# Performance work log

Measured on AMD Instinct MI355X. Metric: run time of the kernel, lower is better.

Reference implementation:

```python
import jax, jax.numpy as jnp
import numpy as np

HIDDEN = 768
HEADS = 12
HEAD_DIM = HIDDEN // HEADS
INTER = 1152
WINDOW = 128
EPS = 1e-5
ROPE_WAVELENGTH = 10000.0


def setup_inputs() -> dict:
    key = jax.random.key(0)
    ks = jax.random.split(key, 8)
    B, S = 2, 2048
    x = jax.random.normal(ks[0], (B, S, HIDDEN), dtype=jnp.float32)
    padding_mask = jnp.ones((B, S), dtype=jnp.int32)
    sc = 0.02
    wqkv = jax.random.normal(ks[1], (HIDDEN, 3 * HIDDEN), dtype=jnp.float32) * sc
    wo_attn = jax.random.normal(ks[2], (HIDDEN, HIDDEN), dtype=jnp.float32) * sc
    wi0 = jax.random.normal(ks[3], (HIDDEN, INTER), dtype=jnp.float32) * sc
    wi1 = jax.random.normal(ks[4], (HIDDEN, INTER), dtype=jnp.float32) * sc
    wo_mlp = jax.random.normal(ks[5], (INTER, HIDDEN), dtype=jnp.float32) * sc
    g_attn = jnp.ones((HIDDEN,), dtype=jnp.float32)
    g_mlp = jnp.ones((HIDDEN,), dtype=jnp.float32)
    return dict(x=x, padding_mask=padding_mask, wqkv=wqkv, wo_attn=wo_attn,
                wi0=wi0, wi1=wi1, wo_mlp=wo_mlp, g_attn=g_attn, g_mlp=g_mlp)


def _rmsnorm(x, gamma):
    # Keras LayerNormalization(rms_scaling=True): x * rsqrt(mean(x^2)+eps) * gamma
    inv = jax.lax.rsqrt(jnp.mean(jnp.square(x), axis=-1, keepdims=True) + EPS)
    return x * inv * gamma


def _rope(t):
    # t: [B, S, H, D]; standard rotate-half RoPE over the head dim
    S, D = t.shape[1], t.shape[3]
    inv_freq = 1.0 / (ROPE_WAVELENGTH ** (jnp.arange(0, D, 2, dtype=jnp.float32) / D))
    freqs = jnp.arange(S, dtype=jnp.float32)[:, None] * inv_freq[None, :]  # [S, D/2]
    emb = jnp.concatenate([freqs, freqs], axis=-1)  # [S, D]
    cos = jnp.cos(emb)[None, :, None, :]
    sin = jnp.sin(emb)[None, :, None, :]
    h1, h2 = jnp.split(t, 2, axis=-1)
    rot = jnp.concatenate([-h2, h1], axis=-1)
    return t * cos + rot * sin


def reference(x, padding_mask, wqkv, wo_attn, wi0, wi1, wo_mlp, g_attn, g_mlp):
    B, S, _ = x.shape
    # --- attention sub-block ---
    res = x
    h = _rmsnorm(x, g_attn)
    qkv = (h @ wqkv).reshape(B, S, 3, HEADS, HEAD_DIM)
    q, k, v = qkv[:, :, 0], qkv[:, :, 1], qkv[:, :, 2]  # [B, S, H, D]
    q = _rope(q)
    k = _rope(k)
    scores = jnp.einsum('bqhd,bkhd->bhqk', q, k) / jnp.sqrt(
        jnp.asarray(HEAD_DIM, x.dtype))
    pos = jnp.arange(S)
    window = (jnp.abs(pos[:, None] - pos[None, :]) <= WINDOW // 2).astype(jnp.float32)
    mask = window[None, None, :, :] * padding_mask.astype(jnp.float32)[:, None, None, :]
    scores = scores + (1.0 - mask) * -1e9
    attn = jax.nn.softmax(scores, axis=-1)
    out = jnp.einsum('bhqk,bkhd->bqhd', attn, v).reshape(B, S, HIDDEN)
    x = res + out @ wo_attn
    # --- GeGLU MLP sub-block ---
    res = x
    h = _rmsnorm(x, g_mlp)
    h = jax.nn.gelu(h @ wi0, approximate=True) * (h @ wi1)
    return res + h @ wo_mlp
```

## Files before the change

kernel.cpp:

```cpp
#include <hip/hip_runtime.h>
#include <hip/hip_bf16.h>

#define HID 768
#define NHEADS 12
#define HD 64
#define INTER 1152
#define SEQ 2048
#define NB 2
#define ROWS (NB * SEQ)
#define QTA 64
#define KTA 192

typedef __attribute__((ext_vector_type(8))) short bf16x8;
typedef __attribute__((ext_vector_type(4))) float f32x4;

__device__ __forceinline__ float bf2f(unsigned short u) {
    union { unsigned int i; float f; } c; c.i = ((unsigned int)u) << 16; return c.f;
}
__device__ __forceinline__ unsigned short f2bf(float f) {
    union { float f; unsigned int i; } c; c.f = f;
    unsigned int b = c.i;
    b += 0x7FFFu + ((b >> 16) & 1u);
    return (unsigned short)(b >> 16);
}
__device__ __forceinline__ void gload16(const void* g, void* l) {
    __builtin_amdgcn_global_load_lds((const __attribute__((address_space(1))) unsigned int*)g,
                                     (__attribute__((address_space(3))) unsigned int*)l,
                                     16, 0, 0);
}

__device__ __forceinline__ void wt_tile(const float* __restrict__ W,
                                        unsigned short* __restrict__ Wt,
                                        int K, int N, int bx, int by,
                                        float (*t)[33]) {
    int tx = threadIdx.x & 31, ty = threadIdx.x >> 5;
    #pragma unroll
    for (int i = 0; i < 4; ++i)
        t[ty + i * 8][tx] = W[(size_t)(by * 32 + ty + i * 8) * N + bx * 32 + tx];
    __syncthreads();
    #pragma unroll
    for (int i = 0; i < 4; ++i)
        Wt[(size_t)(bx * 32 + ty + i * 8) * K + by * 32 + tx] = f2bf(t[tx][ty + i * 8]);
}

__global__ __launch_bounds__(256) void prep_rms_kernel(const float* __restrict__ x,
                                                       const float* __restrict__ g,
                                                       unsigned short* __restrict__ hbf,
                                                       const float* __restrict__ wqkv,
                                                       const float* __restrict__ woa,
                                                       const float* __restrict__ wi0,
                                                       const float* __restrict__ wi1,
                                                       const float* __restrict__ wom,
                                                       unsigned short* __restrict__ wqkvT,
                                                       unsigned short* __restrict__ woaT,
                                                       unsigned short* __restrict__ wi0T,
                                                       unsigned short* __restrict__ wi1T,
                                                       unsigned short* __restrict__ womT,
                                                       float2* __restrict__ rtab) {
    __shared__ float t[32][33];
    __shared__ float red[4];
    int id = blockIdx.x;
    int tid = threadIdx.x;
    if (id < 4096) {
        const float* xr = x + (size_t)id * HID;
        unsigned short* orow = hbf + (size_t)id * HID;
        float v0 = xr[tid], v1 = xr[tid + 256], v2 = xr[tid + 512];
        float s = v0 * v0 + v1 * v1 + v2 * v2;
        #pragma unroll
        for (int m = 32; m >= 1; m >>= 1) s += __shfl_xor(s, m, 64);
        if ((tid & 63) == 0) red[tid >> 6] = s;
        __syncthreads();
        float tot = red[0] + red[1] + red[2] + red[3];
        float inv = rsqrtf(tot * (1.0f / HID) + 1e-5f);
        orow[tid]       = f2bf(v0 * inv * g[tid]);
        orow[tid + 256] = f2bf(v1 * inv * g[tid + 256]);
        orow[tid + 512] = f2bf(v2 * inv * g[tid + 512]);
        return;
    }
    id -= 4096;
    if (id < 1728)       wt_tile(wqkv, wqkvT, 768, 2304, id % 72, id / 72, t);
    else if (id < 2304)  { id -= 1728; wt_tile(woa, woaT, 768, 768, id % 24, id / 24, t); }
    else if (id < 3168)  { id -= 2304; wt_tile(wi0, wi0T, 768, 1152, id % 36, id / 36, t); }
    else if (id < 4032)  { id -= 3168; wt_tile(wi1, wi1T, 768, 1152, id % 36, id / 36, t); }
    else if (id < 4896)  { id -= 4032; wt_tile(wom, womT, 1152, 768, id % 24, id / 24, t); }
    else {
        int idx = (id - 4896) * 256 + tid;
        int s = idx >> 5, fi = idx & 31;
        float ang = (float)s * exp2f(-(float)fi * 0.41524101186f);
        float sn, cs;
        sincosf(ang, &sn, &cs);
        rtab[idx] = make_float2(cs, sn);
    }
}

__global__ __launch_bounds__(256) void rmsnorm_kernel(const float* __restrict__ x,
                                                      const float* __restrict__ g,
                                                      unsigned short* __restrict__ out) {
    int row = blockIdx.x;
    const float* xr = x + (size_t)row * HID;
    unsigned short* orow = out + (size_t)row * HID;
    int tid = threadIdx.x;
    float v0 = xr[tid], v1 = xr[tid + 256], v2 = xr[tid + 512];
    float s = v0 * v0 + v1 * v1 + v2 * v2;
    #pragma unroll
    for (int m = 32; m >= 1; m >>= 1) s += __shfl_xor(s, m, 64);
    __shared__ float red[4];
    if ((tid & 63) == 0) red[tid >> 6] = s;
    __syncthreads();
    float tot = red[0] + red[1] + red[2] + red[3];
    float inv = rsqrtf(tot * (1.0f / HID) + 1e-5f);
    orow[tid]       = f2bf(v0 * inv * g[tid]);
    orow[tid + 256] = f2bf(v1 * inv * g[tid + 256]);
    orow[tid + 512] = f2bf(v2 * inv * g[tid + 512]);
}

__global__ __launch_bounds__(256) void mfma_gemm64(const unsigned short* __restrict__ A,
                                                   const unsigned short* __restrict__ Bt,
                                                   const float* __restrict__ resid,
                                                   float* __restrict__ C,
                                                   int N, int K, int nbx) {
    __shared__ unsigned short As[64 * 128];
    __shared__ unsigned short Bs[64 * 128];
    int nwg = gridDim.x;
    int bid = blockIdx.x;
    int id2 = (bid & 7) * (nwg >> 3) + (bid >> 3);
    int row0 = (id2 / nbx) * 64, col0 = (id2 % nbx) * 64;
    int tid = threadIdx.x;
    int wave = tid >> 6, lane = tid & 63;
    int wr = wave >> 1, wc = wave & 1;
    int fr = lane & 15, fq = lane >> 4;

    const size_t strideA = (size_t)K * 2;
    const char* Ab = (const char*)A;
    const char* Bb = (const char*)Bt;

    f32x4 acc[2][2];
    #pragma unroll
    for (int m = 0; m < 2; ++m)
        #pragma unroll
        for (int n = 0; n < 2; ++n)
            acc[m][n] = (f32x4){0.f, 0.f, 0.f, 0.f};

    int nt = K >> 7;
    for (int t = 0; t < nt; ++t) {
        int k0 = t << 7;
        #pragma unroll
        for (int r = 0; r < 4; ++r) {
            int L = r * 4096 + tid * 16;
            int row = L >> 8;
            int ss = ((L >> 4) & 15) ^ (row & 15);
            gload16(Ab + (size_t)(row0 + row) * strideA + (size_t)k0 * 2 + ss * 16,
                    (char*)As + L);
            gload16(Bb + (size_t)(col0 + row) * strideA + (size_t)k0 * 2 + ss * 16,
                    (char*)Bs + L);
        }
        __syncthreads();
        #pragma unroll
        for (int kk = 0; kk < 4; ++kk) {
            bf16x8 af[2], bff[2];
            #pragma unroll
            for (int m = 0; m < 2; ++m) {
                int rowa = wr * 32 + m * 16 + fr;
                af[m] = *(const bf16x8*)&As[rowa * 128 + (((kk * 4 + fq)) ^ (rowa & 15)) * 8];
                int rowb = wc * 32 + m * 16 + fr;
                bff[m] = *(const bf16x8*)&Bs[rowb * 128 + (((kk * 4 + fq)) ^ (rowb & 15)) * 8];
            }
            #pragma unroll
            for (int m = 0; m < 2; ++m)
                #pragma unroll
                for (int n = 0; n < 2; ++n)
                    acc[m][n] = __builtin_amdgcn_mfma_f32_16x16x32_bf16(af[m], bff[n], acc[m][n], 0, 0, 0);
        }
        __syncthreads();
    }

    #pragma unroll
    for (int m = 0; m < 2; ++m) {
        #pragma unroll
        for (int j = 0; j < 4; ++j) {
            size_t r = (size_t)(row0 + wr * 32 + m * 16 + fq * 4 + j);
            #pragma unroll
            for (int n = 0; n < 2; ++n) {
                size_t idx = r * N + (col0 + wc * 32 + n * 16 + fr);
                float v = acc[m][n][j];
                if (resid) v += resid[idx];
                C[idx] = v;
            }
        }
    }
}

__global__ __launch_bounds__(256) void gemm_qkv128(const unsigned short* __restrict__ A,
                                                   const unsigned short* __restrict__ Bt,
                                                   const float2* __restrict__ rtab,
                                                   unsigned short* __restrict__ Qb,
                                                   unsigned short* __restrict__ Kb,
                                                   unsigned short* __restrict__ Vt) {
    __shared__ unsigned short As[128 * 128];
    __shared__ unsigned short Bs[64 * 128];
    int bid = blockIdx.x;
    int id2 = (bid & 7) * 144 + (bid >> 3);
    int col0 = (id2 % 36) * 64, row0 = (id2 / 36) * 128;
    int tid = threadIdx.x;
    int wave = tid >> 6, lane = tid & 63;
    int fr = lane & 15, fq = lane >> 4;
    int type = col0 / 768;
    int h = (col0 % 768) >> 6;
    int b = row0 >> 11;
    int s0 = row0 & 2047;
    int bh = b * NHEADS + h;

    const size_t strideA = (size_t)768 * 2;
    const char* Ab = (const char*)A;
    const char* Bb = (const char*)Bt;

    f32x4 acc[2][4];
    #pragma unroll
    for (int m = 0; m < 2; ++m)
        #pragma unroll
        for (int n = 0; n < 4; ++n)
            acc[m][n] = (f32x4){0.f, 0.f, 0.f, 0.f};

    for (int t = 0; t < 6; ++t) {
        int k0 = t << 7;
        #pragma unroll
        for (int r = 0; r < 8; ++r) {
            int L = r * 4096 + tid * 16;
            int row = L >> 8;
            int ss = ((L >> 4) & 15) ^ (row & 15);
            gload16(Ab + (size_t)(row0 + row) * strideA + (size_t)k0 * 2 + ss * 16,
                    (char*)As + L);
        }
        #pragma unroll
        for (int r = 0; r < 4; ++r) {
            int L = r * 4096 + tid * 16;
            int row = L >> 8;
            int ss = ((L >> 4) & 15) ^ (row & 15);
            gload16(Bb + (size_t)(col0 + row) * strideA + (size_t)k0 * 2 + ss * 16,
                    (char*)Bs + L);
        }
        __syncthreads();
        #pragma unroll
        for (int kk = 0; kk < 4; ++kk) {
            bf16x8 af[2], bf[4];
            #pragma unroll
            for (int m = 0; m < 2; ++m) {
                int rowa = wave * 32 + m * 16 + fr;
                af[m] = *(const bf16x8*)&As[rowa * 128 + ((kk * 4 + fq) ^ (rowa & 15)) * 8];
            }
            #pragma unroll
            for (int n = 0; n < 4; ++n) {
                int rowb = n * 16 + fr;
                bf[n] = *(const bf16x8*)&Bs[rowb * 128 + ((kk * 4 + fq) ^ (rowb & 15)) * 8];
            }
            #pragma unroll
            for (int m = 0; m < 2; ++m)
                #pragma unroll
                for (int n = 0; n < 4; ++n)
                    acc[m][n] = __builtin_amdgcn_mfma_f32_16x16x32_bf16(af[m], bf[n], acc[m][n], 0, 0, 0);
        }
        __syncthreads();
    }

    if (type < 2) {
        unsigned short* P = (type == 0 ? Qb : Kb) + ((size_t)bh * SEQ) * 64;
        #pragma unroll
        for (int m = 0; m < 2; ++m)
            #pragma unroll
            for (int n = 0; n < 4; ++n) {
                int d = n * 16 + fr;
                int fi = d & 31;
                #pragma unroll
                for (int j = 0; j < 4; ++j) {
                    int s = s0 + wave * 32 + m * 16 + fq * 4 + j;
                    float2 cs = rtab[s * 32 + fi];
                    float val = acc[m][n][j], par = acc[m][n ^ 2][j];
                    float o = (d < 32) ? val * cs.x - par * cs.y
                                       : val * cs.x + par * cs.y;
                    P[(size_t)s * 64 + d] = f2bf(o);
                }
            }
    } else {
        unsigned short* vt = As;
        #pragma unroll
        for (int m = 0; m < 2; ++m)
            #pragma unroll
            for (int n = 0; n < 4; ++n) {
                int d = n * 16 + fr;
                #pragma unroll
                for (int j = 0; j < 4; ++j)
                    vt[d * 136 + wave * 32 + m * 16 + fq * 4 + j] = f2bf(acc[m][n][j]);
            }
        __syncthreads();
        int d = tid >> 2, sg = tid & 3;
        unsigned short* vrow = Vt + ((size_t)bh * 64 + d) * SEQ + s0 + sg * 32;
        #pragma unroll
        for (int i = 0; i < 4; ++i)
            *(bf16x8*)(vrow + i * 8) = *(const bf16x8*)&vt[d * 136 + sg * 32 + i * 8];
    }
}

__global__ __launch_bounds__(256) void gemm_ffn128(const unsigned short* __restrict__ A,
                                                   const unsigned short* __restrict__ B0t,
                                                   const unsigned short* __restrict__ B1t,
                                                   unsigned short* __restrict__ O) {
    __shared__ unsigned short As[128 * 64];
    __shared__ unsigned short Bs0[64 * 64];
    __shared__ unsigned short Bs1[64 * 64];
    int bid = blockIdx.x;
    int id2 = (bid & 7) * 72 + (bid >> 3);
    int col0 = (id2 % 18) * 64, row0 = (id2 / 18) * 128;
    int tid = threadIdx.x;
    int wave = tid >> 6, lane = tid & 63;
    int fr = lane & 15, fq = lane >> 4;

    f32x4 acc0[2][4], acc1[2][4];
    #pragma unroll
    for (int m = 0; m < 2; ++m)
        #pragma unroll
        for (int n = 0; n < 4; ++n) {
            acc0[m][n] = (f32x4){0.f, 0.f, 0.f, 0.f};
            acc1[m][n] = (f32x4){0.f, 0.f, 0.f, 0.f};
        }

    const size_t strideA = (size_t)768 * 2;
    const char* Ab  = (const char*)A;
    const char* B0b = (const char*)B0t;
    const char* B1b = (const char*)B1t;

    for (int k0 = 0; k0 < 768; k0 += 64) {
        #pragma unroll
        for (int r = 0; r < 4; ++r) {
            int L = r * 4096 + tid * 16;
            int row = L >> 7;
            int ss = ((L >> 4) & 7) ^ (row & 7);
            gload16(Ab + (size_t)(row0 + row) * strideA + (size_t)k0 * 2 + ss * 16,
                    (char*)As + L);
        }
        #pragma unroll
        for (int r = 0; r < 2; ++r) {
            int L = r * 4096 + tid * 16;
            int row = L >> 7;
            int ss = ((L >> 4) & 7) ^ (row & 7);
            size_t goff = (size_t)(col0 + row) * strideA + (size_t)k0 * 2 + ss * 16;
            gload16(B0b + goff, (char*)Bs0 + L);
            gload16(B1b + goff, (char*)Bs1 + L);
        }
        __syncthreads();
        #pragma unroll
        for (int kk = 0; kk < 2; ++kk) {
            bf16x8 af[2], b0[4], b1[4];
            #pragma unroll
            for (int m = 0; m < 2; ++m) {
                int rowa = wave * 32 + m * 16 + fr;
                af[m] = *(const bf16x8*)&As[rowa * 64 + ((kk * 4 + fq) ^ (rowa & 7)) * 8];
            }
            #pragma unroll
            for (int n = 0; n < 4; ++n) {
                int rowb = n * 16 + fr;
                int sl = ((kk * 4 + fq) ^ (rowb & 7)) * 8;
                b0[n] = *(const bf16x8*)&Bs0[rowb * 64 + sl];
                b1[n] = *(const bf16x8*)&Bs1[rowb * 64 + sl];
            }
            #pragma unroll
            for (int m = 0; m < 2; ++m)
                #pragma unroll
                for (int n = 0; n < 4; ++n) {
                    acc0[m][n] = __builtin_amdgcn_mfma_f32_16x16x32_bf16(af[m], b0[n], acc0[m][n], 0, 0, 0);
                    acc1[m][n] = __builtin_amdgcn_mfma_f32_16x16x32_bf16(af[m], b1[n], acc1[m][n], 0, 0, 0);
                }
        }
        __syncthreads();
    }

    #pragma unroll
    for (int m = 0; m < 2; ++m)
        #pragma unroll
        for (int n = 0; n < 4; ++n)
            #pragma unroll
            for (int j = 0; j < 4; ++j) {
                int r = row0 + wave * 32 + m * 16 + fq * 4 + j;
                float xa = acc0[m][n][j];
                float tn = tanhf(0.7978845608028654f * (xa + 0.044715f * xa * xa * xa));
                float gv = 0.5f * xa * (1.f + tn) * acc1[m][n][j];
                O[(size_t)r * INTER + col0 + n * 16 + fr] = f2bf(gv);
            }
}

__global__ __launch_bounds__(256) void attn_mfma(const unsigned short* __restrict__ Qb,
                                                 const unsigned short* __restrict__ Kb,
                                                 const unsigned short* __restrict__ Vt,
                                                 const int* __restrict__ pmask,
                                                 unsigned short* __restrict__ ao) {
    __shared__ unsigned short Ks[KTA * 64];
    __shared__ unsigned short Vs[64 * KTA];
    __shared__ unsigned short Ps[4][16 * KTA];
    __shared__ float pmsk[KTA];

    int bid = blockIdx.x;
    int qt = bid & 31;
    int h  = (bid >> 5) % NHEADS;
    int b  = bid / (32 * NHEADS);
    int bh = b * NHEADS + h;
    int q0 = qt * QTA;
    int kstart = q0 - 64;
    int tid = threadIdx.x;
    int wave = tid >> 6, lane = tid & 63;
    int fr = lane & 15, fq = lane >> 4;

    const unsigned short* Kg = Kb + ((size_t)bh * SEQ) * 64;
    const unsigned short* Vg = Vt + ((size_t)bh * 64) * SEQ;

    const unsigned short* Qg = Qb + ((size_t)bh * SEQ + q0 + wave * 16 + fr) * 64 + fq * 8;
    bf16x8 qf0 = *(const bf16x8*)(Qg);
    bf16x8 qf1 = *(const bf16x8*)(Qg + 32);
    if (tid < KTA) {
        int k = kstart + tid;
        pmsk[tid] = (k >= 0 && k < SEQ) ? (1.0f - (float)pmask[b * SEQ + k]) * -1e9f
                                        : -1e9f;
    }

    bool interior = (qt != 0) && (qt != 31);
    if (interior) {
        #pragma unroll
        for (int r = 0; r < 6; ++r) {
            int c = r * 256 + tid;
            int row = c >> 3, slot = c & 7;
            int ss = slot ^ (row & 7);
            gload16(Kg + (size_t)(kstart + row) * 64 + ss * 8, (char*)Ks + c * 16);
        }
        #pragma unroll
        for (int r = 0; r < 6; ++r) {
            int c = r * 256 + tid;
            int d = c / 24, slot = c - d * 24;
            int ss = (slot & ~7) | ((slot & 7) ^ (d & 7));
            gload16(Vg + (size_t)d * SEQ + kstart + ss * 8, (char*)Vs + c * 16);
        }
    } else {
        #pragma unroll
        for (int r = 0; r < 6; ++r) {
            int c = r * 256 + tid;
            int row = c >> 3, slot = c & 7;
            int ss = slot ^ (row & 7);
            int sk = kstart + row;
            bf16x8 val = {0, 0, 0, 0, 0, 0, 0, 0};
            if (sk >= 0 && sk < SEQ)
                val = *(const bf16x8*)(Kg + (size_t)sk * 64 + ss * 8);
            *(bf16x8*)((char*)Ks + c * 16) = val;
        }
        #pragma unroll
        for (int r = 0; r < 6; ++r) {
            int c = r * 256 + tid;
            int d = c / 24, slot = c - d * 24;
            int ss = (slot & ~7) | ((slot & 7) ^ (d & 7));
            int start = kstart + ss * 8;
            bf16x8 val = {0, 0, 0, 0, 0, 0, 0, 0};
            if (start >= 0 && start + 8 <= SEQ)
                val = *(const bf16x8*)(Vg + (size_t)d * SEQ + start);
            *(bf16x8*)((char*)Vs + c * 16) = val;
        }
    }
    __syncthreads();

    f32x4 sc[12];
    #pragma unroll
    for (int n = 0; n < 12; ++n) sc[n] = (f32x4){0.f, 0.f, 0.f, 0.f};
    #pragma unroll
    for (int n = 0; n < 12; ++n) {
        int row = n * 16 + fr;
        int base = row * 64;
        bf16x8 k0 = *(const bf16x8*)&Ks[base + ((fq)     ^ (row & 7)) * 8];
        bf16x8 k1 = *(const bf16x8*)&Ks[base + ((4 + fq) ^ (row & 7)) * 8];
        sc[n] = __builtin_amdgcn_mfma_f32_16x16x32_bf16(qf0, k0, sc[n], 0, 0, 0);
        sc[n] = __builtin_amdgcn_mfma_f32_16x16x32_bf16(qf1, k1, sc[n], 0, 0, 0);
    }

    int qrow_base = q0 + wave * 16 + fq * 4;
    float mj[4] = {-1e30f, -1e30f, -1e30f, -1e30f}, sj[4];
    #pragma unroll
    for (int n = 0; n < 12; ++n) {
        int k = kstart + n * 16 + fr;
        float pm = pmsk[n * 16 + fr];
        #pragma unroll
        for (int j = 0; j < 4; ++j) {
            int diff = qrow_base + j - k;
            float s = sc[n][j] * 0.125f + pm;
            if (diff > 64 || diff < -64) s = -1e30f;
            sc[n][j] = s;
            mj[j] = fmaxf(mj[j], s);
        }
    }
    #pragma unroll
    for (int j = 0; j < 4; ++j) {
        #pragma unroll
        for (int mk = 1; mk < 16; mk <<= 1)
            mj[j] = fmaxf(mj[j], __shfl_xor(mj[j], mk, 16));
        sj[j] = 0.f;
    }
    #pragma unroll
    for (int n = 0; n < 12; ++n)
        #pragma unroll
        for (int j = 0; j < 4; ++j) {
            float e = expf(sc[n][j] - mj[j]);
            sc[n][j] = e;
            sj[j] += e;
        }
    #pragma unroll
    for (int j = 0; j < 4; ++j)
        #pragma unroll
        for (int mk = 1; mk < 16; mk <<= 1)
            sj[j] += __shfl_xor(sj[j], mk, 16);

    unsigned short* Pw = Ps[wave];
    #pragma unroll
    for (int n = 0; n < 12; ++n) {
        int slot = n * 2 + (fr >> 3);
        #pragma unroll
        for (int j = 0; j < 4; ++j) {
            int row = fq * 4 + j;
            int ss = (slot & ~7) | ((slot & 7) ^ (row & 7));
            Pw[row * KTA + ss * 8 + (fr & 7)] = f2bf(sc[n][j]);
        }
    }

    f32x4 oacc[4];
    #pragma unroll
    for (int n = 0; n < 4; ++n) oacc[n] = (f32x4){0.f, 0.f, 0.f, 0.f};
    #pragma unroll
    for (int kt = 0; kt < 6; ++kt) {
        int slot = kt * 4 + fq;
        int ssp = (slot & ~7) | ((slot & 7) ^ (fr & 7));
        bf16x8 pa = *(const bf16x8*)&Pw[fr * KTA + ssp * 8];
        #pragma unroll
        for (int n = 0; n < 4; ++n) {
            int d = n * 16 + fr;
            int ssv = (slot & ~7) | ((slot & 7) ^ (d & 7));
            bf16x8 vf = *(const bf16x8*)&Vs[d * KTA + ssv * 8];
            oacc[n] = __builtin_amdgcn_mfma_f32_16x16x32_bf16(pa, vf, oacc[n], 0, 0, 0);
        }
    }

    unsigned short* aob = ao + ((size_t)(b * SEQ + qrow_base)) * HID + h * 64;
    float rs[4];
    #pragma unroll
    for (int j = 0; j < 4; ++j) rs[j] = 1.0f / sj[j];
    #pragma unroll
    for (int n = 0; n < 4; ++n)
        #pragma unroll
        for (int j = 0; j < 4; ++j)
            aob[(size_t)j * HID + n * 16 + fr] = f2bf(oacc[n][j] * rs[j]);
}

extern "C" void kernel_launch(void* const* d_in, const int* in_sizes, int n_in,
                              void* d_out, int out_size, void* d_ws, size_t ws_size,
                              hipStream_t stream) {
    const float* x       = (const float*)d_in[0];
    const int*   pmask   = (const int*)d_in[1];
    const float* wqkv    = (const float*)d_in[2];
    const float* wo_attn = (const float*)d_in[3];
    const float* wi0     = (const float*)d_in[4];
    const float* wi1     = (const float*)d_in[5];
    const float* wo_mlp  = (const float*)d_in[6];
    const float* g_attn  = (const float*)d_in[7];
    const float* g_mlp   = (const float*)d_in[8];
    float* out = (float*)d_out;

    char* w = (char*)d_ws;
    unsigned short* hbf   = (unsigned short*)(w);
    unsigned short* aobf  = (unsigned short*)(w + 6291456);
    unsigned short* Qb    = (unsigned short*)(w + 12582912);
    unsigned short* Kb    = (unsigned short*)(w + 18874368);
    unsigned short* Vt    = (unsigned short*)(w + 25165824);
    unsigned short* mgate = (unsigned short*)(w + 31457280);
    float2*         rtab  = (float2*)(w + 40894464);
    unsigned short* wqkvT = (unsigned short*)(w + 41418752);
    unsigned short* woaT  = (unsigned short*)(w + 44957696);
    unsigned short* wi0T  = (unsigned short*)(w + 46137344);
    unsigned short* wi1T  = (unsigned short*)(w + 47906816);
    unsigned short* womT  = (unsigned short*)(w + 49676288);

    prep_rms_kernel<<<4096 + 5152, 256, 0, stream>>>(x, g_attn, hbf,
                                                     wqkv, wo_attn, wi0, wi1, wo_mlp,
                                                     wqkvT, woaT, wi0T, wi1T, womT, rtab);
    gemm_qkv128<<<1152, 256, 0, stream>>>(hbf, wqkvT, rtab, Qb, Kb, Vt);
    attn_mfma<<<NB * NHEADS * (SEQ / QTA), 256, 0, stream>>>(Qb, Kb, Vt, pmask, aobf);
    mfma_gemm64<<<768, 256, 0, stream>>>(aobf, woaT, x, out, 768, 768, 12);
    rmsnorm_kernel<<<ROWS, 256, 0, stream>>>(out, g_mlp, hbf);
    gemm_ffn128<<<576, 256, 0, stream>>>(hbf, wi0T, wi1T, mgate);
    mfma_gemm64<<<768, 256, 0, stream>>>(mgate, womT, out, out, 768, 1152, 12);
}
```

Before: 122.5 us.

## Use 128-row output GEMM tiles and skip out-of-window key tiles in attention

The two output-projection GEMMs switch from 64x64 tiles with 768 blocks to 128x64 tiles with 384 blocks. Each wave now computes 32x64, which reuses B fragments and halves grid size, at the cost of lower occupancy and fewer blocks per CU. In attention, each wave computes QK scores only for the 9 key tiles that can fall inside its sliding window instead of all 12, and reuses the K shared buffer for P to cut LDS use. This adds a barrier and zero-fill stores, and the PV loop drops from 6 to 5 k-steps.

```diff
diff --git a/kernel.cpp b/kernel.cpp
--- a/kernel.cpp
+++ b/kernel.cpp
@@ -14,9 +14,6 @@
 typedef __attribute__((ext_vector_type(8))) short bf16x8;
 typedef __attribute__((ext_vector_type(4))) float f32x4;
 
-__device__ __forceinline__ float bf2f(unsigned short u) {
-    union { unsigned int i; float f; } c; c.i = ((unsigned int)u) << 16; return c.f;
-}
 __device__ __forceinline__ unsigned short f2bf(float f) {
     union { float f; unsigned int i; } c; c.f = f;
     unsigned int b = c.i;
@@ -114,80 +111,86 @@
     orow[tid + 512] = f2bf(v2 * inv * g[tid + 512]);
 }
 
-__global__ __launch_bounds__(256) void mfma_gemm64(const unsigned short* __restrict__ A,
-                                                   const unsigned short* __restrict__ Bt,
-                                                   const float* __restrict__ resid,
-                                                   float* __restrict__ C,
-                                                   int N, int K, int nbx) {
-    __shared__ unsigned short As[64 * 128];
+__global__ __launch_bounds__(256) void gemm_wo128(const unsigned short* __restrict__ A,
+                                                  const unsigned short* __restrict__ Bt,
+                                                  const float* __restrict__ resid,
+                                                  float* __restrict__ C,
+                                                  int N, int K) {
+    __shared__ unsigned short As[128 * 128];
     __shared__ unsigned short Bs[64 * 128];
+    int nbx = N >> 6;
     int nwg = gridDim.x;
     int bid = blockIdx.x;
     int id2 = (bid & 7) * (nwg >> 3) + (bid >> 3);
-    int row0 = (id2 / nbx) * 64, col0 = (id2 % nbx) * 64;
+    int col0 = (id2 % nbx) * 64, row0 = (id2 / nbx) * 128;
     int tid = threadIdx.x;
     int wave = tid >> 6, lane = tid & 63;
-    int wr = wave >> 1, wc = wave & 1;
     int fr = lane & 15, fq = lane >> 4;
 
     const size_t strideA = (size_t)K * 2;
     const char* Ab = (const char*)A;
     const char* Bb = (const char*)Bt;
 
-    f32x4 acc[2][2];
+    f32x4 acc[2][4];
     #pragma unroll
     for (int m = 0; m < 2; ++m)
         #pragma unroll
-        for (int n = 0; n < 2; ++n)
+        for (int n = 0; n < 4; ++n)
             acc[m][n] = (f32x4){0.f, 0.f, 0.f, 0.f};
 
     int nt = K >> 7;
     for (int t = 0; t < nt; ++t) {
         int k0 = t << 7;
         #pragma unroll
-        for (int r = 0; r < 4; ++r) {
+        for (int r = 0; r < 8; ++r) {
             int L = r * 4096 + tid * 16;
             int row = L >> 8;
             int ss = ((L >> 4) & 15) ^ (row & 15);
             gload16(Ab + (size_t)(row0 + row) * strideA + (size_t)k0 * 2 + ss * 16,
                     (char*)As + L);
+        }
+        #pragma unroll
+        for (int r = 0; r < 4; ++r) {
+            int L = r * 4096 + tid * 16;
+            int row = L >> 8;
+            int ss = ((L >> 4) & 15) ^ (row & 15);
             gload16(Bb + (size_t)(col0 + row) * strideA + (size_t)k0 * 2 + ss * 16,
                     (char*)Bs + L);
         }
         __syncthreads();
         #pragma unroll
         for (int kk = 0; kk < 4; ++kk) {
-            bf16x8 af[2], bff[2];
+            bf16x8 af[2], bf[4];
             #pragma unroll
             for (int m = 0; m < 2; ++m) {
-                int rowa = wr * 32 + m * 16 + fr;
-                af[m] = *(const bf16x8*)&As[rowa * 128 + (((kk * 4 + fq)) ^ (rowa & 15)) * 8];
-                int rowb = wc * 32 + m * 16 + fr;
-                bff[m] = *(const bf16x8*)&Bs[rowb * 128 + (((kk * 4 + fq)) ^ (rowb & 15)) * 8];
+                int rowa = wave * 32 + m * 16 + fr;
+                af[m] = *(const bf16x8*)&As[rowa * 128 + ((kk * 4 + fq) ^ (rowa & 15)) * 8];
+            }
+            #pragma unroll
+            for (int n = 0; n < 4; ++n) {
+                int rowb = n * 16 + fr;
+                bf[n] = *(const bf16x8*)&Bs[rowb * 128 + ((kk * 4 + fq) ^ (rowb & 15)) * 8];
             }
             #pragma unroll
             for (int m = 0; m < 2; ++m)
                 #pragma unroll
-                for (int n = 0; n < 2; ++n)
-                    acc[m][n] = __builtin_amdgcn_mfma_f32_16x16x32_bf16(af[m], bff[n], acc[m][n], 0, 0, 0);
-        }
-        __syncthreads();
-    }
-
-    #pragma unroll
-    for (int m = 0; m < 2; ++m) {
+                for (int n = 0; n < 4; ++n)
+                    acc[m][n] = __builtin_amdgcn_mfma_f32_16x16x32_bf16(af[m], bf[n], acc[m][n], 0, 0, 0);
+        }
+        __syncthreads();
+    }
+
+    #pragma unroll
+    for (int m = 0; m < 2; ++m)
         #pragma unroll
         for (int j = 0; j < 4; ++j) {
-            size_t r = (size_t)(row0 + wr * 32 + m * 16 + fq * 4 + j);
-            #pragma unroll
-            for (int n = 0; n < 2; ++n) {
-                size_t idx = r * N + (col0 + wc * 32 + n * 16 + fr);
-                float v = acc[m][n][j];
-                if (resid) v += resid[idx];
-                C[idx] = v;
-            }
-        }
-    }
+            size_t r = (size_t)(row0 + wave * 32 + m * 16 + fq * 4 + j);
+            #pragma unroll
+            for (int n = 0; n < 4; ++n) {
+                size_t idx = r * N + (col0 + n * 16 + fr);
+                C[idx] = acc[m][n][j] + resid[idx];
+            }
+        }
 }
 
 __global__ __launch_bounds__(256) void gemm_qkv128(const unsigned short* __restrict__ A,
@@ -394,7 +397,6 @@
                                                  unsigned short* __restrict__ ao) {
     __shared__ unsigned short Ks[KTA * 64];
     __shared__ unsigned short Vs[64 * KTA];
-    __shared__ unsigned short Ps[4][16 * KTA];
     __shared__ float pmsk[KTA];
 
     int bid = blockIdx.x;
@@ -462,31 +464,32 @@
     }
     __syncthreads();
 
-    f32x4 sc[12];
-    #pragma unroll
-    for (int n = 0; n < 12; ++n) sc[n] = (f32x4){0.f, 0.f, 0.f, 0.f};
-    #pragma unroll
-    for (int n = 0; n < 12; ++n) {
-        int row = n * 16 + fr;
+    f32x4 sc[9];
+    #pragma unroll
+    for (int ni = 0; ni < 9; ++ni) sc[ni] = (f32x4){0.f, 0.f, 0.f, 0.f};
+    #pragma unroll
+    for (int ni = 0; ni < 9; ++ni) {
+        int row = (wave + ni) * 16 + fr;
         int base = row * 64;
         bf16x8 k0 = *(const bf16x8*)&Ks[base + ((fq)     ^ (row & 7)) * 8];
         bf16x8 k1 = *(const bf16x8*)&Ks[base + ((4 + fq) ^ (row & 7)) * 8];
-        sc[n] = __builtin_amdgcn_mfma_f32_16x16x32_bf16(qf0, k0, sc[n], 0, 0, 0);
-        sc[n] = __builtin_amdgcn_mfma_f32_16x16x32_bf16(qf1, k1, sc[n], 0, 0, 0);
+        sc[ni] = __builtin_amdgcn_mfma_f32_16x16x32_bf16(qf0, k0, sc[ni], 0, 0, 0);
+        sc[ni] = __builtin_amdgcn_mfma_f32_16x16x32_bf16(qf1, k1, sc[ni], 0, 0, 0);
     }
 
     int qrow_base = q0 + wave * 16 + fq * 4;
     float mj[4] = {-1e30f, -1e30f, -1e30f, -1e30f}, sj[4];
     #pragma unroll
-    for (int n = 0; n < 12; ++n) {
-        int k = kstart + n * 16 + fr;
-        float pm = pmsk[n * 16 + fr];
+    for (int ni = 0; ni < 9; ++ni) {
+        int kp = (wave + ni) * 16 + fr;
+        int k = kstart + kp;
+        float pm = pmsk[kp];
         #pragma unroll
         for (int j = 0; j < 4; ++j) {
             int diff = qrow_base + j - k;
-            float s = sc[n][j] * 0.125f + pm;
+            float s = sc[ni][j] * 0.125f + pm;
             if (diff > 64 || diff < -64) s = -1e30f;
-            sc[n][j] = s;
+            sc[ni][j] = s;
             mj[j] = fmaxf(mj[j], s);
         }
     }
@@ -498,11 +501,11 @@
         sj[j] = 0.f;
     }
     #pragma unroll
-    for (int n = 0; n < 12; ++n)
+    for (int ni = 0; ni < 9; ++ni)
         #pragma unroll
         for (int j = 0; j < 4; ++j) {
-            float e = expf(sc[n][j] - mj[j]);
-            sc[n][j] = e;
+            float e = expf(sc[ni][j] - mj[j]);
+            sc[ni][j] = e;
             sj[j] += e;
         }
     #pragma unroll
@@ -511,24 +514,39 @@
         for (int mk = 1; mk < 16; mk <<= 1)
             sj[j] += __shfl_xor(sj[j], mk, 16);
 
-    unsigned short* Pw = Ps[wave];
-    #pragma unroll
-    for (int n = 0; n < 12; ++n) {
+    __syncthreads();
+
+    unsigned short* Pw = Ks + wave * 16 * KTA;
+    #pragma unroll
+    for (int ni = 0; ni < 9; ++ni) {
+        int n = wave + ni;
         int slot = n * 2 + (fr >> 3);
         #pragma unroll
         for (int j = 0; j < 4; ++j) {
             int row = fq * 4 + j;
             int ss = (slot & ~7) | ((slot & 7) ^ (row & 7));
-            Pw[row * KTA + ss * 8 + (fr & 7)] = f2bf(sc[n][j]);
+            Pw[row * KTA + ss * 8 + (fr & 7)] = f2bf(sc[ni][j]);
+        }
+    }
+    #pragma unroll
+    for (int n = 0; n < 12; ++n) {
+        if (n >= wave && n <= wave + 8) continue;
+        int slot = n * 2 + (fr >> 3);
+        #pragma unroll
+        for (int j = 0; j < 4; ++j) {
+            int row = fq * 4 + j;
+            int ss = (slot & ~7) | ((slot & 7) ^ (row & 7));
+            Pw[row * KTA + ss * 8 + (fr & 7)] = 0;
         }
     }
 
     f32x4 oacc[4];
     #pragma unroll
     for (int n = 0; n < 4; ++n) oacc[n] = (f32x4){0.f, 0.f, 0.f, 0.f};
-    #pragma unroll
-    for (int kt = 0; kt < 6; ++kt) {
-        int slot = kt * 4 + fq;
+    int kt0 = wave >> 1;
+    #pragma unroll
+    for (int ki = 0; ki < 5; ++ki) {
+        int slot = (kt0 + ki) * 4 + fq;
         int ssp = (slot & ~7) | ((slot & 7) ^ (fr & 7));
         bf16x8 pa = *(const bf16x8*)&Pw[fr * KTA + ssp * 8];
         #pragma unroll
@@ -584,8 +602,8 @@
                                                      wqkvT, woaT, wi0T, wi1T, womT, rtab);
     gemm_qkv128<<<1152, 256, 0, stream>>>(hbf, wqkvT, rtab, Qb, Kb, Vt);
     attn_mfma<<<NB * NHEADS * (SEQ / QTA), 256, 0, stream>>>(Qb, Kb, Vt, pmask, aobf);
-    mfma_gemm64<<<768, 256, 0, stream>>>(aobf, woaT, x, out, 768, 768, 12);
+    gemm_wo128<<<384, 256, 0, stream>>>(aobf, woaT, x, out, 768, 768);
     rmsnorm_kernel<<<ROWS, 256, 0, stream>>>(out, g_mlp, hbf);
     gemm_ffn128<<<576, 256, 0, stream>>>(hbf, wi0T, wi1T, mgate);
-    mfma_gemm64<<<768, 256, 0, stream>>>(mgate, womT, out, out, 768, 1152, 12);
-}
+    gemm_wo128<<<384, 256, 0, stream>>>(mgate, womT, out, out, 768, 1152);
+}
```

Result: faster. 115.3 us (-5.9%).
